# Kernel tuning notes

Measured on AMD Instinct MI355X. Metric: run time of the kernel, lower is better.

Reference implementation:

```python
import jax, jax.numpy as jnp
import numpy as np

IOU_THR = 0.0  # module calls batched NMS with iou_threshold=0.0


def setup_inputs() -> dict:
    key = jax.random.key(0)
    kx, kc, kr = jax.random.split(key, 3)
    return {
        "x": jax.random.normal(kx, (10,), jnp.float32),
        "c": jax.random.normal(kc, (4,), jnp.float32),   # learned param
        "r": jax.random.normal(kr, (10,), jnp.float32),  # learned param
    }


def _pairwise_iou(b):
    # b: [n,4] (x1,y1,x2,y2); torchvision-style IoU (area not clamped, inter clamped at 0)
    x1, y1, x2, y2 = b[:, 0], b[:, 1], b[:, 2], b[:, 3]
    area = (x2 - x1) * (y2 - y1)
    iw = jnp.maximum(jnp.minimum(x2[:, None], x2[None, :]) - jnp.maximum(x1[:, None], x1[None, :]), 0.0)
    ih = jnp.maximum(jnp.minimum(y2[:, None], y2[None, :]) - jnp.maximum(y1[:, None], y1[None, :]), 0.0)
    inter = iw * ih
    return inter / (area[:, None] + area[None, :] - inter)


def _nms(boxes, scores, thr):
    # returns (order, keep_mask_in_sorted_order), fixed shapes (jit-safe)
    n = boxes.shape[0]
    order = jnp.argsort(-scores)
    iou = _pairwise_iou(boxes[order])
    j = jnp.arange(n)

    def body(i, keep):
        sup = (iou[i] > thr) & keep[i] & (j > i)
        return keep & ~sup

    keep = jax.lax.fori_loop(0, n, body, jnp.ones((n,), bool))
    return order, keep


def reference(x, c, r):
    boxes = jnp.outer(x, c)                      # [10,4]
    scores = r * x                               # [10]
    # batched-NMS coordinate trick: idxs = arange -> each box in its own class
    max_coord = boxes.max()
    offsets = jnp.arange(boxes.shape[0], dtype=boxes.dtype) * (max_coord + 1.0)
    boxes_nms = boxes + offsets[:, None]
    order, keep = _nms(boxes_nms, scores, IOU_THR)
    # torch returns boxes[keep] (dynamic shape). With distinct class ids all boxes
    # survive; we return fixed-shape [10,4] in keep order, suppressed rows zeroed.
    return jnp.where(keep[:, None], boxes[order], 0.0)
```

## Files before the change

### kernel.cpp

```cpp
#include <hip/hip_runtime.h>
#include <math.h>

#define N 10
#define C 4

__global__ __launch_bounds__(64, 1)
void Model_78056735637556_kernel(const float* __restrict__ x,
                                 const float* __restrict__ c,
                                 const float* __restrict__ r,
                                 float* __restrict__ out) {
    __shared__ float s_boxes[N][C];
    __shared__ float s_scores[N];
    __shared__ int   s_order[N];
    __shared__ int   s_keep[N];
    __shared__ float s_n[N][5];

    const int t = threadIdx.x;
    const int i = t >> 2;
    const int k = t & 3;

    if (t < N * C) s_boxes[i][k] = x[i] * c[k];
    if (t < N) { s_scores[t] = r[t] * x[t]; s_keep[t] = 1; }
    __syncthreads();

    if (t < N) {
        const float s = s_scores[t];
        int rank = 0;
        #pragma unroll
        for (int j = 0; j < N; ++j) {
            const float sj = s_scores[j];
            rank += (sj > s) || ((sj == s) && (j < t));
        }
        s_order[rank] = t;
    }
    __syncthreads();

    float n0 = 0.0f, n1 = 0.0f, n2 = 0.0f, n3 = 0.0f, ar = 0.0f;
    if (t < N) {
        float m = -INFINITY;
        #pragma unroll
        for (int ii = 0; ii < N; ++ii)
            #pragma unroll
            for (int kk = 0; kk < C; ++kk)
                m = fmaxf(m, s_boxes[ii][kk]);
        const float off = m + 1.0f;

        const int o = s_order[t];
        const float d = (float)o * off;
        n0 = s_boxes[o][0] + d;
        n1 = s_boxes[o][1] + d;
        n2 = s_boxes[o][2] + d;
        n3 = s_boxes[o][3] + d;
        ar = (n2 - n0) * (n3 - n1);
        s_n[t][0] = n0; s_n[t][1] = n1; s_n[t][2] = n2; s_n[t][3] = n3;
        s_n[t][4] = ar;
    }
    __syncthreads();

    #pragma unroll
    for (int p = 0; p < N - 1; ++p) {
        if (t > p && t < N) {
            if (s_keep[p] && s_keep[t]) {
                const float iw = fmaxf(fminf(s_n[p][2], n2) - fmaxf(s_n[p][0], n0), 0.0f);
                const float ih = fmaxf(fminf(s_n[p][3], n3) - fmaxf(s_n[p][1], n1), 0.0f);
                const float inter = iw * ih;
                const float iou = inter / (s_n[p][4] + ar - inter);
                if (iou > 0.0f) s_keep[t] = 0;
            }
        }
        __syncthreads();
    }

    if (t < N * C) {
        out[t] = s_keep[i] ? s_boxes[s_order[i]][k] : 0.0f;
    }
}

extern "C" void kernel_launch(void* const* d_in, const int* in_sizes, int n_in,
                              void* d_out, int out_size, void* d_ws, size_t ws_size,
                              hipStream_t stream) {
    const float* x = (const float*)d_in[0];
    const float* c = (const float*)d_in[1];
    const float* r = (const float*)d_in[2];
    float* out = (float*)d_out;
    Model_78056735637556_kernel<<<1, 64, 0, stream>>>(x, c, r, out);
}
```

Before: 59.37 us.

## Compute all NMS pairwise IoUs in parallel with bitmask suppression

After: 57.89 us. 1.03x faster.

```diff
diff --git a/kernel.cpp b/kernel.cpp
--- a/kernel.cpp
+++ b/kernel.cpp
@@ -3,6 +3,7 @@
 
 #define N 10
 #define C 4
+#define NPAIR 45
 
 __global__ __launch_bounds__(64, 1)
 void Model_78056735637556_kernel(const float* __restrict__ x,
@@ -12,15 +13,16 @@
     __shared__ float s_boxes[N][C];
     __shared__ float s_scores[N];
     __shared__ int   s_order[N];
-    __shared__ int   s_keep[N];
-    __shared__ float s_n[N][5];
+    __shared__ int   s_mask[N];
+    __shared__ float s_off;
 
     const int t = threadIdx.x;
-    const int i = t >> 2;
-    const int k = t & 3;
 
-    if (t < N * C) s_boxes[i][k] = x[i] * c[k];
-    if (t < N) { s_scores[t] = r[t] * x[t]; s_keep[t] = 1; }
+    if (t < N * C) {
+        const int i = t >> 2, k = t & 3;
+        s_boxes[i][k] = x[i] * c[k];
+    }
+    if (t < N) { s_scores[t] = r[t] * x[t]; s_mask[t] = 0; }
     __syncthreads();
 
     if (t < N) {
@@ -33,46 +35,69 @@
         }
         s_order[rank] = t;
     }
-    __syncthreads();
-
-    float n0 = 0.0f, n1 = 0.0f, n2 = 0.0f, n3 = 0.0f, ar = 0.0f;
-    if (t < N) {
+    if (t == N) {
         float m = -INFINITY;
         #pragma unroll
         for (int ii = 0; ii < N; ++ii)
             #pragma unroll
             for (int kk = 0; kk < C; ++kk)
                 m = fmaxf(m, s_boxes[ii][kk]);
-        const float off = m + 1.0f;
-
-        const int o = s_order[t];
-        const float d = (float)o * off;
-        n0 = s_boxes[o][0] + d;
-        n1 = s_boxes[o][1] + d;
-        n2 = s_boxes[o][2] + d;
-        n3 = s_boxes[o][3] + d;
-        ar = (n2 - n0) * (n3 - n1);
-        s_n[t][0] = n0; s_n[t][1] = n1; s_n[t][2] = n2; s_n[t][3] = n3;
-        s_n[t][4] = ar;
+        s_off = m + 1.0f;
     }
     __syncthreads();
 
-    #pragma unroll
-    for (int p = 0; p < N - 1; ++p) {
-        if (t > p && t < N) {
-            if (s_keep[p] && s_keep[t]) {
-                const float iw = fmaxf(fminf(s_n[p][2], n2) - fmaxf(s_n[p][0], n0), 0.0f);
-                const float ih = fmaxf(fminf(s_n[p][3], n3) - fmaxf(s_n[p][1], n1), 0.0f);
-                const float inter = iw * ih;
-                const float iou = inter / (s_n[p][4] + ar - inter);
-                if (iou > 0.0f) s_keep[t] = 0;
-            }
+    if (t < NPAIR) {
+        int p = 0, j = 1, acc = 0;
+        #pragma unroll
+        for (int pp = 0; pp < N - 1; ++pp) {
+            const int cnt = N - 1 - pp;
+            const bool in = (t >= acc) && (t < acc + cnt);
+            p = in ? pp : p;
+            j = in ? (pp + 1 + (t - acc)) : j;
+            acc += cnt;
         }
-        __syncthreads();
+
+        const float off = s_off;
+        const int op = s_order[p];
+        const int oj = s_order[j];
+        const float dp = (float)op * off;
+        const float dj = (float)oj * off;
+
+        const float p0 = s_boxes[op][0] + dp, p1 = s_boxes[op][1] + dp;
+        const float p2 = s_boxes[op][2] + dp, p3 = s_boxes[op][3] + dp;
+        const float q0 = s_boxes[oj][0] + dj, q1 = s_boxes[oj][1] + dj;
+        const float q2 = s_boxes[oj][2] + dj, q3 = s_boxes[oj][3] + dj;
+
+        const float ap = (p2 - p0) * (p3 - p1);
+        const float aq = (q2 - q0) * (q3 - q1);
+
+        const float iw = fmaxf(fminf(p2, q2) - fmaxf(p0, q0), 0.0f);
+        const float ih = fmaxf(fminf(p3, q3) - fmaxf(p1, q1), 0.0f);
+        const float inter = iw * ih;
+        const float iou = inter / (ap + aq - inter);
+
+        if (iou > 0.0f)
+            atomicOr(&s_mask[p], 1 << j);
     }
+    __syncthreads();
+
+    const int m0 = s_mask[0], m1 = s_mask[1], m2 = s_mask[2], m3 = s_mask[3];
+    const int m4 = s_mask[4], m5 = s_mask[5], m6 = s_mask[6], m7 = s_mask[7];
+    const int m8 = s_mask[8];
+    int keep = (1 << N) - 1;
+    if (keep & (1 << 0)) keep &= ~m0;
+    if (keep & (1 << 1)) keep &= ~m1;
+    if (keep & (1 << 2)) keep &= ~m2;
+    if (keep & (1 << 3)) keep &= ~m3;
+    if (keep & (1 << 4)) keep &= ~m4;
+    if (keep & (1 << 5)) keep &= ~m5;
+    if (keep & (1 << 6)) keep &= ~m6;
+    if (keep & (1 << 7)) keep &= ~m7;
+    if (keep & (1 << 8)) keep &= ~m8;
 
     if (t < N * C) {
-        out[t] = s_keep[i] ? s_boxes[s_order[i]][k] : 0.0f;
+        const int i = t >> 2, k = t & 3;
+        out[t] = ((keep >> i) & 1) ? s_boxes[s_order[i]][k] : 0.0f;
     }
 }
 
```
